# Kernel tuning notes

Hardware: AMD Instinct MI355X
Metric: run time of the kernel (lower is better)

## Reference

```python
import jax, jax.numpy as jnp
import numpy as np

B, C, H, W = 16, 3, 768, 768
K = 21


def setup_inputs() -> dict:
    key = jax.random.key(0)
    k1, k2 = jax.random.split(key)
    inp = jax.random.normal(k1, (B, C, H, W), dtype=jnp.float32)
    kernel = jax.random.uniform(k2, (B, K, K), dtype=jnp.float32)
    return {"input": inp, "kernel": kernel}


def reference(input, kernel):
    # input: [B, C, H, W]; kernel: [B, k, k] (one blur kernel per sample)
    b = input.shape[0]
    k = kernel.shape[-1]
    p = k // 2  # k=21 is odd -> symmetric reflection pad
    x = jnp.pad(input, ((0, 0), (0, 0), (p, p), (p, p)), mode="reflect")
    # Match torch: conv2d(input_pad.transpose(0,1), kernel.unsqueeze(1), groups=B)
    # lhs: [C, B, Hp, Wp] (channels-as-batch), rhs: [B, 1, k, k], groups=B
    x = jnp.transpose(x, (1, 0, 2, 3))
    w = kernel[:, None, :, :]
    y = jax.lax.conv_general_dilated(
        x, w,
        window_strides=(1, 1),
        padding="VALID",
        dimension_numbers=("NCHW", "OIHW", "NCHW"),
        feature_group_count=b,
    )
    return jnp.transpose(y, (1, 0, 2, 3))  # [B, C, H, W]
```

## Files before the change

### kernel.cpp

```cpp
#include <hip/hip_runtime.h>

#define KS   21
#define HALO 10
#define TH   16
#define TW   256
#define PH   (TH + 2*HALO)
#define PW   (TW + 2*HALO)
#define HDIM 768

__device__ __forceinline__ int reflect_idx(int x, int n) {
    if (x < 0) x = -x;
    if (x >= n) x = 2 * n - 2 - x;
    return x;
}

__global__ __launch_bounds__(256, 3)
void blur_by_kernel(const float* __restrict__ in,
                    const float* __restrict__ kern,
                    float* __restrict__ out) {
    __shared__ float tile[PH * PW];

    const int bx  = blockIdx.x;
    const int by  = blockIdx.y;
    const int bc  = blockIdx.z;
    const int b   = bc / 3;
    const int tid = threadIdx.x;
    const int lane = tid & 63;
    const int w    = tid >> 6;

    const float* plane = in + (size_t)bc * (HDIM * HDIM);
    const int y0 = by * TH - HALO;
    const int x0 = bx * TW - HALO;

    for (int idx = tid; idx < PH * PW; idx += 256) {
        int r = idx / PW;
        int c = idx - r * PW;
        tile[idx] = plane[reflect_idx(y0 + r, HDIM) * HDIM + reflect_idx(x0 + c, HDIM)];
    }
    __syncthreads();

    const float* kb = kern + b * (KS * KS);

    float acc[4][4] = {};
    float4 x4[6];
    const float* xs = (const float*)x4;
    const int colbase = lane * 4;

    #define LOADROW(t)                                                        \
        {                                                                     \
            const float4* lrow = (const float4*)&tile[(w * 4 + (t)) * PW + colbase]; \
            _Pragma("unroll")                                                 \
            for (int j = 0; j < 6; ++j) x4[j] = lrow[j];                      \
        }

    #define FMAROW(r, ki)                                                     \
        {                                                                     \
            const float* krow = kb + (ki) * KS;                               \
            _Pragma("unroll")                                                 \
            for (int kj = 0; kj < KS; ++kj) {                                 \
                float kv = krow[kj];                                          \
                _Pragma("unroll")                                             \
                for (int c = 0; c < 4; ++c)                                   \
                    acc[r][c] = fmaf(kv, xs[kj + c], acc[r][c]);              \
            }                                                                 \
        }

    #pragma unroll
    for (int t = 0; t < 3; ++t) {
        LOADROW(t);
        #pragma unroll
        for (int r = 0; r < 4; ++r)
            if (t - r >= 0) FMAROW(r, t - r);
    }

    for (int t = 3; t <= 20; ++t) {
        LOADROW(t);
        #pragma unroll
        for (int r = 0; r < 4; ++r)
            FMAROW(r, t - r);
    }

    #pragma unroll
    for (int t = 21; t < 24; ++t) {
        LOADROW(t);
        #pragma unroll
        for (int r = 0; r < 4; ++r)
            if (t - r <= 20) FMAROW(r, t - r);
    }

    float* oplane = out + (size_t)bc * (HDIM * HDIM);
    const int gx = bx * TW + colbase;
    const int gy = by * TH + w * 4;
    #pragma unroll
    for (int r = 0; r < 4; ++r) {
        float4 v = make_float4(acc[r][0], acc[r][1], acc[r][2], acc[r][3]);
        *(float4*)&oplane[(size_t)(gy + r) * HDIM + gx] = v;
    }
}

extern "C" void kernel_launch(void* const* d_in, const int* in_sizes, int n_in,
                              void* d_out, int out_size, void* d_ws, size_t ws_size,
                              hipStream_t stream) {
    const float* in   = (const float*)d_in[0];
    const float* kern = (const float*)d_in[1];
    float* out = (float*)d_out;

    dim3 grid(HDIM / TW, HDIM / TH, 16 * 3);
    dim3 block(256);
    blur_by_kernel<<<grid, block, 0, stream>>>(in, kern, out);
}
```

Measured before the change: 423.7 us.

## Compute six output rows per thread with double-buffered register row loads

Raises the tile height to 24 rows so each wavefront computes 6 output rows instead of 4. Each loaded input row is now reused across more accumulator rows, which cuts LDS reads per output and shrinks the halo share of the tile. Row loads alternate between two register buffers so the next row's LDS read can overlap the current row's FMAs. The main loop is kept rolled to limit code size. The cost is more accumulator and buffer registers and a larger shared tile, which may lower occupancy.

```diff
diff --git a/kernel.cpp b/kernel.cpp
--- a/kernel.cpp
+++ b/kernel.cpp
@@ -2,10 +2,11 @@
 
 #define KS   21
 #define HALO 10
-#define TH   16
+#define TH   24
 #define TW   256
+#define R    6
 #define PH   (TH + 2*HALO)
-#define PW   (TW + 2*HALO)
+#define PW   276
 #define HDIM 768
 
 __device__ __forceinline__ int reflect_idx(int x, int n) {
@@ -41,58 +42,69 @@
 
     const float* kb = kern + b * (KS * KS);
 
-    float acc[4][4] = {};
-    float4 x4[6];
-    const float* xs = (const float*)x4;
+    float acc[R][4] = {};
+    float4 xA[6], xB[6];
     const int colbase = lane * 4;
 
-    #define LOADROW(t)                                                        \
-        {                                                                     \
-            const float4* lrow = (const float4*)&tile[(w * 4 + (t)) * PW + colbase]; \
-            _Pragma("unroll")                                                 \
-            for (int j = 0; j < 6; ++j) x4[j] = lrow[j];                      \
+    #define LOADROW(buf, t)                                                    \
+        {                                                                      \
+            const float4* lrow = (const float4*)&tile[(w * R + (t)) * PW + colbase]; \
+            _Pragma("unroll")                                                  \
+            for (int j = 0; j < 6; ++j) buf[j] = lrow[j];                      \
         }
 
-    #define FMAROW(r, ki)                                                     \
-        {                                                                     \
+    #define FMAROW(buf, r, ki)                                                \
+        {                                                                      \
+            const float* xs_ = (const float*)(buf);                           \
             const float* krow = kb + (ki) * KS;                               \
             _Pragma("unroll")                                                 \
             for (int kj = 0; kj < KS; ++kj) {                                 \
                 float kv = krow[kj];                                          \
                 _Pragma("unroll")                                             \
                 for (int c = 0; c < 4; ++c)                                   \
-                    acc[r][c] = fmaf(kv, xs[kj + c], acc[r][c]);              \
+                    acc[r][c] = fmaf(kv, xs_[kj + c], acc[r][c]);             \
             }                                                                 \
         }
 
-    #pragma unroll
-    for (int t = 0; t < 3; ++t) {
-        LOADROW(t);
-        #pragma unroll
-        for (int r = 0; r < 4; ++r)
-            if (t - r >= 0) FMAROW(r, t - r);
+    #define FMAS_ALL(buf, t)                                                  \
+        {                                                                      \
+            _Pragma("unroll")                                                 \
+            for (int r = 0; r < R; ++r) FMAROW(buf, r, (t) - r);              \
+        }
+
+    #define FMAS_P(buf, t)                                                    \
+        {                                                                      \
+            _Pragma("unroll")                                                 \
+            for (int r = 0; r < R; ++r)                                       \
+                if ((t) - r >= 0 && (t) - r <= KS - 1) FMAROW(buf, r, (t) - r); \
+        }
+
+    LOADROW(xA, 0);
+    LOADROW(xB, 1);  FMAS_P(xA, 0);
+    LOADROW(xA, 2);  FMAS_P(xB, 1);
+    LOADROW(xB, 3);  FMAS_P(xA, 2);
+    LOADROW(xA, 4);  FMAS_P(xB, 3);
+    LOADROW(xB, 5);  FMAS_P(xA, 4);
+
+    #pragma unroll 1
+    for (int t = 5; t < 20; t += 2) {
+        LOADROW(xA, t + 1);
+        FMAS_ALL(xB, t);
+        LOADROW(xB, t + 2);
+        FMAS_ALL(xA, t + 1);
     }
 
-    for (int t = 3; t <= 20; ++t) {
-        LOADROW(t);
-        #pragma unroll
-        for (int r = 0; r < 4; ++r)
-            FMAROW(r, t - r);
-    }
-
-    #pragma unroll
-    for (int t = 21; t < 24; ++t) {
-        LOADROW(t);
-        #pragma unroll
-        for (int r = 0; r < 4; ++r)
-            if (t - r <= 20) FMAROW(r, t - r);
-    }
+    LOADROW(xA, 22); FMAS_P(xB, 21);
+    LOADROW(xB, 23); FMAS_P(xA, 22);
+    LOADROW(xA, 24); FMAS_P(xB, 23);
+    LOADROW(xB, 25); FMAS_P(xA, 24);
+    FMAS_P(xB, 25);
 
     float* oplane = out + (size_t)bc * (HDIM * HDIM);
     const int gx = bx * TW + colbase;
-    const int gy = by * TH + w * 4;
+    const int gy = by * TH + w * R;
     #pragma unroll
-    for (int r = 0; r < 4; ++r) {
+    for (int r = 0; r < R; ++r) {
         float4 v = make_float4(acc[r][0], acc[r][1], acc[r][2], acc[r][3]);
         *(float4*)&oplane[(size_t)(gy + r) * HDIM + gx] = v;
     }
```

New measurement: 428.5 us. About the same (+1.1%).

## Use packed FP32 FMA with paired kernel weights via inline asm

Applied to the files above, without the earlier changes.

Rewrites the inner convolution loop to use v_pk_fma_f32, which processes two output columns per instruction. Odd-offset operand pairs are built with v_pk_mov_b32, and kernel weights are repacked into 64-bit pairs by a small prep kernel so they can be read as scalar operands. The main row loop is no longer unrolled, and the tile row pitch changes. The aim is to halve the FMA instruction count, at the cost of an extra launch and inline-asm constraints that may raise register pressure or block compiler scheduling.

```diff
diff --git a/kernel.cpp b/kernel.cpp
--- a/kernel.cpp
+++ b/kernel.cpp
@@ -4,9 +4,14 @@
 #define HALO 10
 #define TH   16
 #define TW   256
+#define R    4
 #define PH   (TH + 2*HALO)
-#define PW   (TW + 2*HALO)
+#define PW   276
 #define HDIM 768
+#define NPAIR 11
+
+typedef float f32x2 __attribute__((ext_vector_type(2)));
+typedef unsigned long long u64;
 
 __device__ __forceinline__ int reflect_idx(int x, int n) {
     if (x < 0) x = -x;
@@ -14,9 +19,21 @@
     return x;
 }
 
+__global__ void prep_kernel(const float* __restrict__ kern, u64* __restrict__ kws) {
+    int i = blockIdx.x * 256 + threadIdx.x;
+    if (i >= 16 * KS * NPAIR) return;
+    int j   = i % NPAIR;
+    int row = i / NPAIR;
+    const float* kr = kern + row * KS;
+    union { float f[2]; u64 u; } p;
+    p.f[0] = kr[2 * j];
+    p.f[1] = (2 * j + 1 < KS) ? kr[2 * j + 1] : 0.0f;
+    kws[i] = p.u;
+}
+
 __global__ __launch_bounds__(256, 3)
 void blur_by_kernel(const float* __restrict__ in,
-                    const float* __restrict__ kern,
+                    const u64* __restrict__ kws,
                     float* __restrict__ out) {
     __shared__ float tile[PH * PW];
 
@@ -39,30 +56,48 @@
     }
     __syncthreads();
 
-    const float* kb = kern + b * (KS * KS);
+    const u64* kb = kws + b * (KS * NPAIR);
 
-    float acc[4][4] = {};
-    float4 x4[6];
-    const float* xs = (const float*)x4;
+    f32x2 acc[R][2] = {};
+    f32x2 we[12];
+    f32x2 wo[11];
     const int colbase = lane * 4;
 
-    #define LOADROW(t)                                                        \
-        {                                                                     \
-            const float4* lrow = (const float4*)&tile[(w * 4 + (t)) * PW + colbase]; \
-            _Pragma("unroll")                                                 \
-            for (int j = 0; j < 6; ++j) x4[j] = lrow[j];                      \
+    #define LOADROW(t)                                                         \
+        {                                                                      \
+            const float4* lrow = (const float4*)&tile[(w * R + (t)) * PW + colbase]; \
+            _Pragma("unroll")                                                  \
+            for (int j = 0; j < 6; ++j) {                                      \
+                float4 v = lrow[j];                                            \
+                we[2 * j]     = (f32x2){v.x, v.y};                             \
+                we[2 * j + 1] = (f32x2){v.z, v.w};                             \
+            }                                                                  \
+            _Pragma("unroll")                                                  \
+            for (int p = 0; p < 11; ++p)                                       \
+                asm("v_pk_mov_b32 %0, %1, %2 op_sel:[1,0] op_sel_hi:[0,0]"     \
+                    : "=v"(wo[p]) : "v"(we[p]), "v"(we[p + 1]));               \
         }
 
-    #define FMAROW(r, ki)                                                     \
-        {                                                                     \
-            const float* krow = kb + (ki) * KS;                               \
-            _Pragma("unroll")                                                 \
-            for (int kj = 0; kj < KS; ++kj) {                                 \
-                float kv = krow[kj];                                          \
-                _Pragma("unroll")                                             \
-                for (int c = 0; c < 4; ++c)                                   \
-                    acc[r][c] = fmaf(kv, xs[kj + c], acc[r][c]);              \
-            }                                                                 \
+    #define FMAROW(r, ki)                                                      \
+        {                                                                      \
+            const u64* kp = kb + (ki) * NPAIR;                                 \
+            _Pragma("unroll")                                                  \
+            for (int kj = 0; kj < KS; ++kj) {                                  \
+                u64 kv = kp[kj >> 1];                                          \
+                f32x2 xa = (kj & 1) ? wo[kj >> 1]       : we[kj >> 1];         \
+                f32x2 xb = (kj & 1) ? wo[(kj >> 1) + 1] : we[(kj >> 1) + 1];   \
+                if (kj & 1) {                                                  \
+                    asm("v_pk_fma_f32 %0, %1, %2, %0 op_sel:[0,1,0] op_sel_hi:[1,1,1]" \
+                        : "+v"(acc[r][0]) : "v"(xa), "s"(kv));                 \
+                    asm("v_pk_fma_f32 %0, %1, %2, %0 op_sel:[0,1,0] op_sel_hi:[1,1,1]" \
+                        : "+v"(acc[r][1]) : "v"(xb), "s"(kv));                 \
+                } else {                                                       \
+                    asm("v_pk_fma_f32 %0, %1, %2, %0 op_sel:[0,0,0] op_sel_hi:[1,0,1]" \
+                        : "+v"(acc[r][0]) : "v"(xa), "s"(kv));                 \
+                    asm("v_pk_fma_f32 %0, %1, %2, %0 op_sel:[0,0,0] op_sel_hi:[1,0,1]" \
+                        : "+v"(acc[r][1]) : "v"(xb), "s"(kv));                 \
+                }                                                              \
+            }                                                                  \
         }
 
     #pragma unroll
@@ -73,6 +108,7 @@
             if (t - r >= 0) FMAROW(r, t - r);
     }
 
+    #pragma unroll 1
     for (int t = 3; t <= 20; ++t) {
         LOADROW(t);
         #pragma unroll
@@ -90,10 +126,10 @@
 
     float* oplane = out + (size_t)bc * (HDIM * HDIM);
     const int gx = bx * TW + colbase;
-    const int gy = by * TH + w * 4;
+    const int gy = by * TH + w * R;
     #pragma unroll
     for (int r = 0; r < 4; ++r) {
-        float4 v = make_float4(acc[r][0], acc[r][1], acc[r][2], acc[r][3]);
+        float4 v = make_float4(acc[r][0].x, acc[r][0].y, acc[r][1].x, acc[r][1].y);
         *(float4*)&oplane[(size_t)(gy + r) * HDIM + gx] = v;
     }
 }
@@ -104,8 +140,11 @@
     const float* in   = (const float*)d_in[0];
     const float* kern = (const float*)d_in[1];
     float* out = (float*)d_out;
+    u64* kws  = (u64*)d_ws;
+
+    prep_kernel<<<dim3((16 * KS * NPAIR + 255) / 256), dim3(256), 0, stream>>>(kern, kws);
 
     dim3 grid(HDIM / TW, HDIM / TH, 16 * 3);
     dim3 block(256);
-    blur_by_kernel<<<grid, block, 0, stream>>>(in, kern, out);
+    blur_by_kernel<<<grid, block, 0, stream>>>(in, kws, out);
 }
```

After: 399.7 us. 5.7% less time.
